# Kernel optimization log

Hardware: AMD Instinct MI355X
Metric: run time of the kernel (lower is better)

The kernel has to match this reference:

```python
import jax, jax.numpy as jnp
import numpy as np

EMBED_DIM = 1024
NUM_HEADS = 16
HEAD_DIM = EMBED_DIM // NUM_HEADS
EXPANSION = 4
EPS = 1e-5


def setup_inputs() -> dict:
    key = jax.random.key(0)
    ks = jax.random.split(key, 8)
    D, F = EMBED_DIM, EMBED_DIM * EXPANSION
    s = lambda d: 1.0 / np.sqrt(d)
    return {
        "x": jax.random.normal(ks[0], (8, 1024, D), jnp.float32),
        "qkv_w": jax.random.normal(ks[1], (D, 3 * D), jnp.float32) * s(D),
        "qkv_b": jnp.zeros((3 * D,), jnp.float32),
        "out_w": jax.random.normal(ks[2], (D, D), jnp.float32) * s(D),
        "out_b": jnp.zeros((D,), jnp.float32),
        "ffn_w1": jax.random.normal(ks[3], (D, F), jnp.float32) * s(D),
        "ffn_b1": jnp.zeros((F,), jnp.float32),
        "ffn_w2": jax.random.normal(ks[4], (F, D), jnp.float32) * s(F),
        "ffn_b2": jnp.zeros((D,), jnp.float32),
        "ln1_g": jnp.ones((D,), jnp.float32),
        "ln1_b": jnp.zeros((D,), jnp.float32),
        "ln2_g": jnp.ones((D,), jnp.float32),
        "ln2_b": jnp.zeros((D,), jnp.float32),
    }


def _layernorm(x, g, b):
    mu = jnp.mean(x, axis=-1, keepdims=True)
    var = jnp.mean(jnp.square(x - mu), axis=-1, keepdims=True)
    return (x - mu) * jax.lax.rsqrt(var + EPS) * g + b


def reference(x, qkv_w, qkv_b, out_w, out_b, ffn_w1, ffn_b1, ffn_w2, ffn_b2,
              ln1_g, ln1_b, ln2_g, ln2_b):
    B, N, D = x.shape
    H, Hd = NUM_HEADS, HEAD_DIM
    scale = Hd ** -0.5

    residual = x
    h = _layernorm(x, ln1_g, ln1_b)
    qkv = h @ qkv_w + qkv_b                      # [B, N, 3D]
    q, k, v = jnp.split(qkv, 3, axis=-1)
    # [B, N, D] -> [B, H, N, Hd]
    reshape = lambda t: t.reshape(B, N, H, Hd).transpose(0, 2, 1, 3)
    q, k, v = reshape(q), reshape(k), reshape(v)

    attn = jnp.einsum("bhnd,bhmd->bhnm", q, k) * scale
    attn = jax.nn.softmax(attn, axis=-1)
    o = jnp.einsum("bhnm,bhmd->bhnd", attn, v)   # [B, H, N, Hd]
    o = o.transpose(0, 2, 1, 3).reshape(B, N, D)
    o = o @ out_w + out_b
    x = residual + o

    residual = x
    h = _layernorm(x, ln2_g, ln2_b)
    h = jax.nn.gelu(h @ ffn_w1 + ffn_b1, approximate=False) @ ffn_w2 + ffn_b2
    return residual + h
```

## Files before the change

### kernel.cpp

```cpp
#include <hip/hip_runtime.h>
#include <hip/hip_bf16.h>


typedef float f32x4 __attribute__((ext_vector_type(4)));
typedef float f32x16 __attribute__((ext_vector_type(16)));
typedef short bf16x8 __attribute__((ext_vector_type(8)));

#define DEV __device__ __forceinline__

DEV f32x4 mfma16(bf16x8 a, bf16x8 b, f32x4 c) {
    return __builtin_amdgcn_mfma_f32_16x16x32_bf16(a, b, c, 0, 0, 0);
}

DEV f32x16 mfma32(bf16x8 a, bf16x8 b, f32x16 c) {
    return __builtin_amdgcn_mfma_f32_32x32x16_bf16(a, b, c, 0, 0, 0);
}

DEV ushort f2bf(float f) {
    union { float f; unsigned u; } v; v.f = f;
    unsigned r = v.u + 0x7FFFu + ((v.u >> 16) & 1u);
    return (ushort)(r >> 16);
}

DEV float bf2f(ushort u) {
    union { unsigned u; float f; } v; v.u = (unsigned)u << 16;
    return v.f;
}

DEV unsigned cvtpk(float lo, float hi) {
    unsigned r;
    asm("v_cvt_pk_bf16_f32 %0, %1, %2" : "=v"(r) : "v"(lo), "v"(hi));
    return r;
}

DEV void gload_lds16(const void* g, void* l) {
    __builtin_amdgcn_global_load_lds(
        (const __attribute__((address_space(1))) void*)g,
        (__attribute__((address_space(3))) void*)l, 16, 0, 0);
}

template <int N> DEV void vmwait() {
    asm volatile("s_waitcnt vmcnt(%0)" :: "n"(N) : "memory");
}
DEV void lgkm0() {
    asm volatile("s_waitcnt lgkmcnt(0)" ::: "memory");
}

constexpr float ATT_SCL = 0.18033688011112042f;

__global__ __launch_bounds__(256) void transpose_w_all(
    const float* __restrict__ w0, const float* __restrict__ w1,
    const float* __restrict__ w2, const float* __restrict__ w3,
    ushort* __restrict__ d0, ushort* __restrict__ d1,
    ushort* __restrict__ d2, ushort* __restrict__ d3)
{
    __shared__ float tile[32][33];
    int id = blockIdx.x;
    const float* src; ushort* dst; int K, N, gx;
    if (id < 3072)      { src = w0; dst = d0; K = 1024; N = 3072; gx = 96; }
    else if (id < 4096) { src = w1; dst = d1; K = 1024; N = 1024; gx = 32; id -= 3072; }
    else if (id < 8192) { src = w2; dst = d2; K = 1024; N = 4096; gx = 128; id -= 4096; }
    else                { src = w3; dst = d3; K = 4096; N = 1024; gx = 32; id -= 8192; }
    const int n0 = (id % gx) * 32, k0 = (id / gx) * 32;
    const int tx = threadIdx.x, ty = threadIdx.y;
#pragma unroll
    for (int i = 0; i < 32; i += 8)
        tile[ty + i][tx] = src[(size_t)(k0 + ty + i) * N + n0 + tx];
    __syncthreads();
#pragma unroll
    for (int i = 0; i < 32; i += 8)
        dst[(size_t)(n0 + ty + i) * K + k0 + tx] = f2bf(tile[tx][ty + i]);
}

__global__ __launch_bounds__(256) void transpose_v(
    const ushort* __restrict__ qkvb, ushort* __restrict__ vt)
{
    __shared__ ushort tile[32][33];
    const int b = blockIdx.z >> 4, h = blockIdx.z & 15;
    const int n0 = blockIdx.x * 32, d0 = blockIdx.y * 32;
    const int tx = threadIdx.x, ty = threadIdx.y;
#pragma unroll
    for (int i = 0; i < 32; i += 8)
        tile[ty + i][tx] =
            qkvb[(size_t)(b * 1024 + n0 + ty + i) * 3072 + 2048 + h * 64 + d0 + tx];
    __syncthreads();
#pragma unroll
    for (int i = 0; i < 32; i += 8)
        vt[((size_t)(b * 16 + h) * 64 + d0 + ty + i) * 1024 + n0 + tx] = tile[tx][ty + i];
}

__global__ __launch_bounds__(256) void ln_bf16(
    const float* __restrict__ x, const float* __restrict__ gw,
    const float* __restrict__ bw, ushort* __restrict__ out)
{
    const int row = blockIdx.x;
    const int t = threadIdx.x;
    const float4 v = ((const float4*)(x + (size_t)row * 1024))[t];
    float s  = v.x + v.y + v.z + v.w;
    float s2 = v.x * v.x + v.y * v.y + v.z * v.z + v.w * v.w;
#pragma unroll
    for (int off = 32; off; off >>= 1) {
        s  += __shfl_xor(s, off);
        s2 += __shfl_xor(s2, off);
    }
    __shared__ float red[16];
    const int wave = t >> 6, lane = t & 63;
    if (lane == 0) { red[wave] = s; red[8 + wave] = s2; }
    __syncthreads();
    s  = red[0] + red[1] + red[2] + red[3];
    s2 = red[8] + red[9] + red[10] + red[11];
    const float mean = s * (1.0f / 1024.0f);
    const float var  = s2 * (1.0f / 1024.0f) - mean * mean;
    const float rstd = rsqrtf(var + 1e-5f);
    const float4 gv = ((const float4*)gw)[t];
    const float4 bv = ((const float4*)bw)[t];
    ushort4 o;
    o.x = f2bf((v.x - mean) * rstd * gv.x + bv.x);
    o.y = f2bf((v.y - mean) * rstd * gv.y + bv.y);
    o.z = f2bf((v.z - mean) * rstd * gv.z + bv.z);
    o.w = f2bf((v.w - mean) * rstd * gv.w + bv.w);
    ((ushort4*)out)[(size_t)row * 256 + t] = o;
}

__global__ __launch_bounds__(256) void ln_bf16b(
    const ushort* __restrict__ x, const float* __restrict__ gw,
    const float* __restrict__ bw, ushort* __restrict__ out)
{
    const int row = blockIdx.x;
    const int t = threadIdx.x;
    const ushort4 uv = ((const ushort4*)(x + (size_t)row * 1024))[t];
    float vx = bf2f(uv.x), vy = bf2f(uv.y), vz = bf2f(uv.z), vw = bf2f(uv.w);
    float s  = vx + vy + vz + vw;
    float s2 = vx * vx + vy * vy + vz * vz + vw * vw;
#pragma unroll
    for (int off = 32; off; off >>= 1) {
        s  += __shfl_xor(s, off);
        s2 += __shfl_xor(s2, off);
    }
    __shared__ float red[16];
    const int wave = t >> 6, lane = t & 63;
    if (lane == 0) { red[wave] = s; red[8 + wave] = s2; }
    __syncthreads();
    s  = red[0] + red[1] + red[2] + red[3];
    s2 = red[8] + red[9] + red[10] + red[11];
    const float mean = s * (1.0f / 1024.0f);
    const float var  = s2 * (1.0f / 1024.0f) - mean * mean;
    const float rstd = rsqrtf(var + 1e-5f);
    const float4 gv = ((const float4*)gw)[t];
    const float4 bv = ((const float4*)bw)[t];
    ushort4 o;
    o.x = f2bf((vx - mean) * rstd * gv.x + bv.x);
    o.y = f2bf((vy - mean) * rstd * gv.y + bv.y);
    o.z = f2bf((vz - mean) * rstd * gv.z + bv.z);
    o.w = f2bf((vw - mean) * rstd * gv.w + bv.w);
    ((ushort4*)out)[(size_t)row * 256 + t] = o;
}

template <int BM, int BN, int WM_, int WN_, int EPI>
__global__ __launch_bounds__(512, 2) void gemm4p(
    const ushort* __restrict__ A, const ushort* __restrict__ BT,
    const float* __restrict__ bias, const float* __restrict__ res,
    void* __restrict__ out, int M, int N, int K)
{
    constexpr int BK = 64;
    constexpr int MR = BM / WM_ / 16;
    constexpr int NR = BN / WN_ / 16;
    constexpr int MH = MR / 2;
    constexpr int CM = MH / 2 > 0 ? MH / 2 : 1;
    constexpr int LA = (BM / 2) / 64;
    constexpr int LB = (BN / 2) / 64;
    constexpr int VMN = LA + LB;
    constexpr int ABYTES = BM * BK * 2;
    constexpr int BBYTES = BN * BK * 2;

    extern __shared__ __align__(16) char smem[];
#define ASB(b) (smem + (b) * ABYTES)
#define BSB(b) (smem + 2 * ABYTES + (b) * BBYTES)

    const int tid = threadIdx.x;
    const int wave = tid >> 6, lane = tid & 63;
    const int g = lane >> 4, lr = lane & 15;
    const int wr = wave / WN_, wc = wave % WN_;
    const int akey = (lr & 7) << 4;

    const int gx = gridDim.x;
    const int nwg = gx * gridDim.y;
    int id = blockIdx.y * gx + blockIdx.x;
    id = (id & 7) * (nwg >> 3) + (id >> 3);
    const int m0 = (id / gx) * BM, n0 = (id % gx) * BN;

    const int trow = tid >> 3;
    const int tblk = (tid & 7) ^ (trow & 7);
    const ushort* pA = A  + (size_t)(m0 + trow) * K + tblk * 8;
    const ushort* pB = BT + (size_t)(n0 + trow) * K + tblk * 8;
    const int woff = wave * 1024;

#define STAGE_A(b, h, kt) do { \
    _Pragma("unroll") for (int i = 0; i < LA; ++i) \
        gload_lds16(pA + ((size_t)((h) * (BM / 2) + i * 64)) * K + (size_t)(kt) * 64, \
                    ASB(b) + (h) * (BM / 2) * 128 + i * 8192 + woff); \
} while (0)
#define STAGE_B(b, h, kt) do { \
    _Pragma("unroll") for (int i = 0; i < LB; ++i) \
        gload_lds16(pB + ((size_t)((h) * (BN / 2) + i * 64)) * K + (size_t)(kt) * 64, \
                    BSB(b) + (h) * (BN / 2) * 128 + i * 8192 + woff); \
} while (0)

    bf16x8 af[CM][2], bfr[NR][2];
    f32x4 acc[MR][NR] = {};

#define LOAD_A(b, h, cj) do { \
    const char* rb_ = ASB(b) + ((h) * (BM / 2) + wr * ((BM / 2) / WM_) \
                               + (cj) * CM * 16 + lr) * 128; \
    _Pragma("unroll") for (int cm = 0; cm < CM; ++cm) \
    _Pragma("unroll") for (int kk = 0; kk < 2; ++kk) \
        af[cm][kk] = *(const bf16x8*)(rb_ + cm * 2048 + ((kk * 64 + g * 16) ^ akey)); \
} while (0)
#define LOAD_B(b) do { \
    const char* rb_ = BSB(b) + (wc * (BN / WN_) + lr) * 128; \
    _Pragma("unroll") for (int ni = 0; ni < NR; ++ni) \
    _Pragma("unroll") for (int kk = 0; kk < 2; ++kk) \
        bfr[ni][kk] = *(const bf16x8*)(rb_ + ni * 2048 + ((kk * 64 + g * 16) ^ akey)); \
} while (0)
#define MFMA_PH(h, cj) do { \
    __builtin_amdgcn_s_setprio(1); \
    _Pragma("unroll") for (int cm = 0; cm < CM; ++cm) \
    _Pragma("unroll") for (int ni = 0; ni < NR; ++ni) \
    _Pragma("unroll") for (int kk = 0; kk < 2; ++kk) \
        acc[(h) * MH + (cj) * CM + cm][ni] = \
            mfma16(af[cm][kk], bfr[ni][kk], acc[(h) * MH + (cj) * CM + cm][ni]); \
    __builtin_amdgcn_s_setprio(0); \
} while (0)

    const int NT = K >> 6;

    STAGE_A(0, 0, 0); STAGE_A(0, 1, 0); STAGE_B(0, 0, 0); STAGE_B(0, 1, 0);
    STAGE_B(1, 0, 1);
    STAGE_A(1, 0, 1);
    vmwait<VMN>();
    __builtin_amdgcn_s_barrier();

    for (int kt = 0; kt < NT; ++kt) {
        const int b = kt & 1, nb = b ^ 1;
        LOAD_A(b, 0, 0); LOAD_B(b);
        if (kt + 1 < NT) STAGE_B(nb, 1, kt + 1);
        __builtin_amdgcn_s_barrier(); lgkm0();
        MFMA_PH(0, 0);
        LOAD_A(b, 0, 1);
        if (kt + 1 < NT) STAGE_A(nb, 1, kt + 1);
        __builtin_amdgcn_s_barrier(); lgkm0();
        MFMA_PH(0, 1);
        LOAD_A(b, 1, 0);
        if (kt + 2 < NT) STAGE_B(b, 0, kt + 2);
        __builtin_amdgcn_s_barrier(); lgkm0();
        MFMA_PH(1, 0);
        LOAD_A(b, 1, 1);
        if (kt + 2 < NT) { STAGE_A(b, 0, kt + 2); vmwait<VMN>(); }
        else if (kt + 1 < NT) vmwait<0>();
        __builtin_amdgcn_s_barrier(); lgkm0();
        MFMA_PH(1, 1);
    }

#pragma unroll
    for (int mi = 0; mi < MR; ++mi) {
        const int row0 = m0 + (mi / MH) * (BM / 2) + wr * ((BM / 2) / WM_)
                       + (mi % MH) * 16 + 4 * g;
#pragma unroll
        for (int ni = 0; ni < NR; ++ni) {
            const int col = n0 + wc * (BN / WN_) + ni * 16 + lr;
            const float bv = bias[col];
#pragma unroll
            for (int r = 0; r < 4; ++r) {
                float v = acc[mi][ni][r] + bv;
                const size_t idx = (size_t)(row0 + r) * N + col;
                if constexpr (EPI == 1) {
                    ((ushort*)out)[idx] = f2bf(v + res[idx]);
                } else if constexpr (EPI == 2) {
                    const float u = 1.595769122f * v + 0.071354816f * v * v * v;
                    const float gs = 1.0f / (1.0f + __expf(-u));
                    ((ushort*)out)[idx] = f2bf(v * gs);
                } else if constexpr (EPI == 3) {
                    ((float*)out)[idx] = v + bf2f(((const ushort*)res)[idx]);
                } else {
                    if (col < 1024) v *= ATT_SCL;
                    ((ushort*)out)[idx] = f2bf(v);
                }
            }
        }
    }
#undef STAGE_A
#undef STAGE_B
#undef LOAD_A
#undef LOAD_B
#undef MFMA_PH
#undef ASB
#undef BSB
}

__global__ __launch_bounds__(256) void attn_kernel(
    const ushort* __restrict__ qkv, const ushort* __restrict__ vtb,
    ushort* __restrict__ o)
{
    __shared__ __align__(16) ushort Ks[64 * 64];
    __shared__ __align__(16) ushort Vt[64 * 64];

    const int tid = threadIdx.x;
    const int wave = tid >> 6, lane = tid & 63;
    const int lq = lane & 31;
    const int hi = lane >> 5;
    const int l7 = lane & 7;

    const int hwid = blockIdx.x;
    const int logical = (hwid & 7) * 128 + (hwid >> 3);
    const int bh = logical >> 3, qt = logical & 7;
    const int b = bh >> 4, head = bh & 15;
    const int q0 = qt * 128 + wave * 32;

    const size_t base  = (size_t)b * 1024 * 3072;
    const size_t vbase = (size_t)bh * 64 * 1024;

    union BF8 { bf16x8 v; ushort u[8]; unsigned w[4]; };

    BF8 qf[4];
    {
        const ushort* qrow = qkv + base + (size_t)(q0 + lq) * 3072 + head * 64;
#pragma unroll
        for (int s = 0; s < 4; ++s) {
            *(ushort4*)&qf[s].u[0] = *(const ushort4*)(qrow + 16 * s + 4 * hi);
            *(ushort4*)&qf[s].u[4] = *(const ushort4*)(qrow + 16 * s + 8 + 4 * hi);
        }
    }

    const int sr = tid >> 3, sc = tid & 7;
    const int swz = (sc ^ (sr & 7)) << 3;
    const ushort* kg0 = qkv + base + (size_t)sr * 3072 + 1024 + head * 64 + sc * 8;
    const ushort* kg1 = kg0 + (size_t)32 * 3072;
    const ushort* vg0 = vtb + vbase + (size_t)sr * 1024 + sc * 8;
    const ushort* vg1 = vg0 + (size_t)32 * 1024;
    ushort* ksw0 = Ks + sr * 64 + swz;
    ushort* ksw1 = Ks + (sr + 32) * 64 + swz;
    ushort* vsw0 = Vt + sr * 64 + swz;
    ushort* vsw1 = Vt + (sr + 32) * 64 + swz;

    float l_st = 0.f;
    f32x16 oacc[2] = {};

    for (int kt = 0; kt < 16; ++kt) {
        const int n0 = kt * 64;
        __syncthreads();
        *(bf16x8*)ksw0 = *(const bf16x8*)(kg0 + (size_t)n0 * 3072);
        *(bf16x8*)ksw1 = *(const bf16x8*)(kg1 + (size_t)n0 * 3072);
        *(bf16x8*)vsw0 = *(const bf16x8*)(vg0 + n0);
        *(bf16x8*)vsw1 = *(const bf16x8*)(vg1 + n0);
        __syncthreads();

        f32x16 sacc[2];
#pragma unroll
        for (int kb = 0; kb < 2; ++kb) {
            f32x16 a = {};
            const ushort* krow = Ks + (kb * 32 + lq) * 64;
#pragma unroll
            for (int s = 0; s < 4; ++s) {
                BF8 kf;
                *(ushort4*)&kf.u[0] = *(const ushort4*)(krow + (((2 * s)     ^ l7) << 3) + 4 * hi);
                *(ushort4*)&kf.u[4] = *(const ushort4*)(krow + (((2 * s + 1) ^ l7) << 3) + 4 * hi);
                a = mfma32(kf.v, qf[s].v, a);
            }
            sacc[kb] = a;
        }

        float p0 = 0.f, p1 = 0.f, p2 = 0.f, p3 = 0.f;
#pragma unroll
        for (int kb = 0; kb < 2; ++kb)
#pragma unroll
            for (int r = 0; r < 16; ++r) {
                const float pe = exp2f(sacc[kb][r]);
                sacc[kb][r] = pe;
                if ((r & 3) == 0)      p0 += pe;
                else if ((r & 3) == 1) p1 += pe;
                else if ((r & 3) == 2) p2 += pe;
                else                   p3 += pe;
            }
        float psum = (p0 + p1) + (p2 + p3);
        psum += __shfl_xor(psum, 32);
        l_st += psum;

#pragma unroll
        for (int kb = 0; kb < 2; ++kb) {
            BF8 pf[2];
#pragma unroll
            for (int t = 0; t < 2; ++t)
#pragma unroll
                for (int w = 0; w < 4; ++w)
                    pf[t].w[w] = cvtpk(sacc[kb][8 * t + 2 * w], sacc[kb][8 * t + 2 * w + 1]);
#pragma unroll
            for (int nb = 0; nb < 2; ++nb) {
                const ushort* vrow = Vt + (nb * 32 + lq) * 64;
#pragma unroll
                for (int t = 0; t < 2; ++t) {
                    BF8 vf;
                    const int blk = 4 * kb + 2 * t;
                    *(ushort4*)&vf.u[0] = *(const ushort4*)(vrow + ((blk       ^ l7) << 3) + 4 * hi);
                    *(ushort4*)&vf.u[4] = *(const ushort4*)(vrow + (((blk + 1) ^ l7) << 3) + 4 * hi);
                    oacc[nb] = mfma32(vf.v, pf[t].v, oacc[nb]);
                }
            }
        }
    }

    const float inv = 1.0f / l_st;
    ushort* orow = o + (size_t)(b * 1024 + q0 + lq) * 1024 + head * 64;
#pragma unroll
    for (int nb = 0; nb < 2; ++nb)
#pragma unroll
        for (int u = 0; u < 4; ++u) {
            uint2 wv;
            wv.x = cvtpk(oacc[nb][4 * u] * inv,     oacc[nb][4 * u + 1] * inv);
            wv.y = cvtpk(oacc[nb][4 * u + 2] * inv, oacc[nb][4 * u + 3] * inv);
            *(uint2*)(orow + nb * 32 + 8 * u + 4 * hi) = wv;
        }
}

extern "C" void kernel_launch(void* const* d_in, const int* in_sizes, int n_in,
                              void* d_out, int out_size, void* d_ws, size_t ws_size,
                              hipStream_t stream)
{
    const float* x      = (const float*)d_in[0];
    const float* qkv_w  = (const float*)d_in[1];
    const float* qkv_b  = (const float*)d_in[2];
    const float* out_w  = (const float*)d_in[3];
    const float* out_b  = (const float*)d_in[4];
    const float* ffn_w1 = (const float*)d_in[5];
    const float* ffn_b1 = (const float*)d_in[6];
    const float* ffn_w2 = (const float*)d_in[7];
    const float* ffn_b2 = (const float*)d_in[8];
    const float* ln1_g  = (const float*)d_in[9];
    const float* ln1_b  = (const float*)d_in[10];
    const float* ln2_g  = (const float*)d_in[11];
    const float* ln2_b  = (const float*)d_in[12];

    constexpr size_t MB = 1u << 20;
    char* ws = (char*)d_ws;
    ushort* wt_qkv = (ushort*)(ws + 0 * MB);
    ushort* wt_out = (ushort*)(ws + 6 * MB);
    ushort* wt_f1  = (ushort*)(ws + 8 * MB);
    ushort* wt_f2  = (ushort*)(ws + 16 * MB);
    ushort* x1b    = (ushort*)(ws + 24 * MB);
    ushort* vtb    = (ushort*)(ws + 40 * MB);
    ushort* hbuf   = (ushort*)(ws + 56 * MB);
    ushort* qkvb   = (ushort*)(ws + 72 * MB);
    ushort* obuf   = (ushort*)(ws + 120 * MB);
    ushort* gbuf   = (ushort*)(ws + 72 * MB);

    const dim3 tb(32, 8);
    transpose_w_all<<<12288, tb, 0, stream>>>(
        qkv_w, out_w, ffn_w1, ffn_w2, wt_qkv, wt_out, wt_f1, wt_f2);

    ln_bf16<<<8192, 256, 0, stream>>>(x, ln1_g, ln1_b, hbuf);

    constexpr int LDS_256 = (256 + 256) * 64 * 2 * 2;
    constexpr int LDS_128 = (256 + 128) * 64 * 2 * 2;

    gemm4p<256, 128, 4, 2, 4><<<dim3(24, 32), 512, LDS_128, stream>>>(
        hbuf, wt_qkv, qkv_b, nullptr, qkvb, 8192, 3072, 1024);

    transpose_v<<<dim3(32, 2, 128), tb, 0, stream>>>(qkvb, vtb);

    attn_kernel<<<1024, 256, 0, stream>>>(qkvb, vtb, obuf);

    gemm4p<256, 128, 4, 2, 1><<<dim3(8, 32), 512, LDS_128, stream>>>(
        obuf, wt_out, out_b, x, x1b, 8192, 1024, 1024);

    ln_bf16b<<<8192, 256, 0, stream>>>(x1b, ln2_g, ln2_b, hbuf);

    gemm4p<256, 256, 2, 4, 2><<<dim3(16, 32), 512, LDS_256, stream>>>(
        hbuf, wt_f1, ffn_b1, nullptr, gbuf, 8192, 4096, 1024);

    gemm4p<256, 128, 4, 2, 3><<<dim3(8, 32), 512, LDS_128, stream>>>(
        gbuf, wt_f2, ffn_b2, (const float*)x1b, (float*)d_out, 8192, 1024, 4096);
}
```

Baseline: 330.4 us.

## Process two 32-row query groups per wave in attention kernel

Each wave now handles 64 query rows as two 32-row groups instead of one, so each attention block covers 256 queries and the grid shrinks from 1024 to 512 blocks. Every K and V fragment read from shared memory feeds two MFMAs, halving LDS reads and global K/V tile loads per query. The cost is roughly double the accumulator and P registers, which may lower occupancy, and fewer blocks in flight on the GPU.

Result: slower. 368.9 us (+11.6%).

```diff
diff --git a/kernel.cpp b/kernel.cpp
--- a/kernel.cpp
+++ b/kernel.cpp
@@ -311,23 +311,24 @@
     const int l7 = lane & 7;
 
     const int hwid = blockIdx.x;
-    const int logical = (hwid & 7) * 128 + (hwid >> 3);
-    const int bh = logical >> 3, qt = logical & 7;
+    const int logical = (hwid & 7) * 64 + (hwid >> 3);
+    const int bh = logical >> 2, qt = logical & 3;
     const int b = bh >> 4, head = bh & 15;
-    const int q0 = qt * 128 + wave * 32;
+    const int q0 = qt * 256 + wave * 64;
 
     const size_t base  = (size_t)b * 1024 * 3072;
     const size_t vbase = (size_t)bh * 64 * 1024;
 
     union BF8 { bf16x8 v; ushort u[8]; unsigned w[4]; };
 
-    BF8 qf[4];
-    {
-        const ushort* qrow = qkv + base + (size_t)(q0 + lq) * 3072 + head * 64;
+    BF8 qf[2][4];
+#pragma unroll
+    for (int gq = 0; gq < 2; ++gq) {
+        const ushort* qrow = qkv + base + (size_t)(q0 + gq * 32 + lq) * 3072 + head * 64;
 #pragma unroll
         for (int s = 0; s < 4; ++s) {
-            *(ushort4*)&qf[s].u[0] = *(const ushort4*)(qrow + 16 * s + 4 * hi);
-            *(ushort4*)&qf[s].u[4] = *(const ushort4*)(qrow + 16 * s + 8 + 4 * hi);
+            *(ushort4*)&qf[gq][s].u[0] = *(const ushort4*)(qrow + 16 * s + 4 * hi);
+            *(ushort4*)&qf[gq][s].u[4] = *(const ushort4*)(qrow + 16 * s + 8 + 4 * hi);
         }
     }
 
@@ -342,8 +343,8 @@
     ushort* vsw0 = Vt + sr * 64 + swz;
     ushort* vsw1 = Vt + (sr + 32) * 64 + swz;
 
-    float l_st = 0.f;
-    f32x16 oacc[2] = {};
+    float l0 = 0.f, l1 = 0.f;
+    f32x16 oacc[2][2] = {};
 
     for (int kt = 0; kt < 16; ++kt) {
         const int n0 = kt * 64;
@@ -354,45 +355,50 @@
         *(bf16x8*)vsw1 = *(const bf16x8*)(vg1 + n0);
         __syncthreads();
 
-        f32x16 sacc[2];
+        f32x16 sacc[2][2] = {};
 #pragma unroll
         for (int kb = 0; kb < 2; ++kb) {
-            f32x16 a = {};
             const ushort* krow = Ks + (kb * 32 + lq) * 64;
 #pragma unroll
             for (int s = 0; s < 4; ++s) {
                 BF8 kf;
                 *(ushort4*)&kf.u[0] = *(const ushort4*)(krow + (((2 * s)     ^ l7) << 3) + 4 * hi);
                 *(ushort4*)&kf.u[4] = *(const ushort4*)(krow + (((2 * s + 1) ^ l7) << 3) + 4 * hi);
-                a = mfma32(kf.v, qf[s].v, a);
+                sacc[0][kb] = mfma32(kf.v, qf[0][s].v, sacc[0][kb]);
+                sacc[1][kb] = mfma32(kf.v, qf[1][s].v, sacc[1][kb]);
             }
-            sacc[kb] = a;
         }
 
-        float p0 = 0.f, p1 = 0.f, p2 = 0.f, p3 = 0.f;
-#pragma unroll
-        for (int kb = 0; kb < 2; ++kb)
-#pragma unroll
-            for (int r = 0; r < 16; ++r) {
-                const float pe = exp2f(sacc[kb][r]);
-                sacc[kb][r] = pe;
-                if ((r & 3) == 0)      p0 += pe;
-                else if ((r & 3) == 1) p1 += pe;
-                else if ((r & 3) == 2) p2 += pe;
-                else                   p3 += pe;
-            }
-        float psum = (p0 + p1) + (p2 + p3);
-        psum += __shfl_xor(psum, 32);
-        l_st += psum;
+#pragma unroll
+        for (int gq = 0; gq < 2; ++gq) {
+            float p0 = 0.f, p1 = 0.f, p2 = 0.f, p3 = 0.f;
+#pragma unroll
+            for (int kb = 0; kb < 2; ++kb)
+#pragma unroll
+                for (int r = 0; r < 16; ++r) {
+                    const float pe = exp2f(sacc[gq][kb][r]);
+                    sacc[gq][kb][r] = pe;
+                    if ((r & 3) == 0)      p0 += pe;
+                    else if ((r & 3) == 1) p1 += pe;
+                    else if ((r & 3) == 2) p2 += pe;
+                    else                   p3 += pe;
+                }
+            float psum = (p0 + p1) + (p2 + p3);
+            psum += __shfl_xor(psum, 32);
+            if (gq == 0) l0 += psum; else l1 += psum;
+        }
 
 #pragma unroll
         for (int kb = 0; kb < 2; ++kb) {
-            BF8 pf[2];
-#pragma unroll
-            for (int t = 0; t < 2; ++t)
-#pragma unroll
-                for (int w = 0; w < 4; ++w)
-                    pf[t].w[w] = cvtpk(sacc[kb][8 * t + 2 * w], sacc[kb][8 * t + 2 * w + 1]);
+            BF8 pf[2][2];
+#pragma unroll
+            for (int gq = 0; gq < 2; ++gq)
+#pragma unroll
+                for (int t = 0; t < 2; ++t)
+#pragma unroll
+                    for (int w = 0; w < 4; ++w)
+                        pf[gq][t].w[w] = cvtpk(sacc[gq][kb][8 * t + 2 * w],
+                                               sacc[gq][kb][8 * t + 2 * w + 1]);
 #pragma unroll
             for (int nb = 0; nb < 2; ++nb) {
                 const ushort* vrow = Vt + (nb * 32 + lq) * 64;
@@ -402,23 +408,27 @@
                     const int blk = 4 * kb + 2 * t;
                     *(ushort4*)&vf.u[0] = *(const ushort4*)(vrow + ((blk       ^ l7) << 3) + 4 * hi);
                     *(ushort4*)&vf.u[4] = *(const ushort4*)(vrow + (((blk + 1) ^ l7) << 3) + 4 * hi);
-                    oacc[nb] = mfma32(vf.v, pf[t].v, oacc[nb]);
+                    oacc[0][nb] = mfma32(vf.v, pf[0][t].v, oacc[0][nb]);
+                    oacc[1][nb] = mfma32(vf.v, pf[1][t].v, oacc[1][nb]);
                 }
             }
         }
     }
 
-    const float inv = 1.0f / l_st;
-    ushort* orow = o + (size_t)(b * 1024 + q0 + lq) * 1024 + head * 64;
-#pragma unroll
-    for (int nb = 0; nb < 2; ++nb)
-#pragma unroll
-        for (int u = 0; u < 4; ++u) {
-            uint2 wv;
-            wv.x = cvtpk(oacc[nb][4 * u] * inv,     oacc[nb][4 * u + 1] * inv);
-            wv.y = cvtpk(oacc[nb][4 * u + 2] * inv, oacc[nb][4 * u + 3] * inv);
-            *(uint2*)(orow + nb * 32 + 8 * u + 4 * hi) = wv;
-        }
+#pragma unroll
+    for (int gq = 0; gq < 2; ++gq) {
+        const float inv = 1.0f / (gq == 0 ? l0 : l1);
+        ushort* orow = o + (size_t)(b * 1024 + q0 + gq * 32 + lq) * 1024 + head * 64;
+#pragma unroll
+        for (int nb = 0; nb < 2; ++nb)
+#pragma unroll
+            for (int u = 0; u < 4; ++u) {
+                uint2 wv;
+                wv.x = cvtpk(oacc[gq][nb][4 * u] * inv,     oacc[gq][nb][4 * u + 1] * inv);
+                wv.y = cvtpk(oacc[gq][nb][4 * u + 2] * inv, oacc[gq][nb][4 * u + 3] * inv);
+                *(uint2*)(orow + nb * 32 + 8 * u + 4 * hi) = wv;
+            }
+    }
 }
 
 extern "C" void kernel_launch(void* const* d_in, const int* in_sizes, int n_in,
@@ -466,7 +476,7 @@
 
     transpose_v<<<dim3(32, 2, 128), tb, 0, stream>>>(qkvb, vtb);
 
-    attn_kernel<<<1024, 256, 0, stream>>>(qkvb, vtb, obuf);
+    attn_kernel<<<512, 256, 0, stream>>>(qkvb, vtb, obuf);
 
     gemm4p<256, 128, 4, 2, 1><<<dim3(8, 32), 512, LDS_128, stream>>>(
         obuf, wt_out, out_b, x, x1b, 8192, 1024, 1024);
```
